# Performance work log

Hardware: AMD Instinct MI355X
Metric: run time of the kernel (lower is better)

## Reference

```python
import jax, jax.numpy as jnp
import numpy as np

P_FACTOR = 3.0
EPS = 1e-12  # torch F.normalize eps


def _l2_normalize(x):
    # matches torch.nn.functional.normalize(x, dim=-1): x / max(||x||, eps)
    n = jnp.linalg.norm(x, axis=-1, keepdims=True)
    return x / jnp.maximum(n, EPS)


def setup_inputs() -> dict:
    key = jax.random.key(0)
    k1, k2, k3 = jax.random.split(key, 3)
    N, D, H, C = 8192, 16384, 256, 28
    return {
        "features": jax.random.normal(k1, (N, H), dtype=jnp.float32),
        "ex_features": jax.random.normal(k2, (D, H), dtype=jnp.float32),
        "ex_class_reps": jax.random.normal(k3, (D, C), dtype=jnp.float32),
    }


def reference(features, ex_features, ex_class_reps):
    # cosine similarity: [N, D]
    s = _l2_normalize(features) @ _l2_normalize(ex_features).T
    # power-law activation: |s|^p * sign(s)
    a = jnp.power(jnp.abs(s), P_FACTOR) * jnp.sign(s)
    intensity = a.sum(axis=1)               # [N]
    echo = a @ ex_class_reps                # [N, C]
    return (echo, intensity)
```

## Files before the change

### kernel.cpp

```cpp
#include <hip/hip_runtime.h>
#include <stdint.h>


typedef unsigned short u16;
typedef __bf16 bf16x8 __attribute__((ext_vector_type(8)));
typedef float f32x4 __attribute__((ext_vector_type(4)));
typedef unsigned short u16x4 __attribute__((ext_vector_type(4)));

#define NQ 8192
#define ND 16384
#define NH 256
#define NC 28
#define DCHUNK 2048
#define NDT 32
#define NSLOT 8

__device__ __forceinline__ u16 f2bf(float f) {
  unsigned u = __builtin_bit_cast(unsigned, f);
  u += 0x7fffu + ((u >> 16) & 1u);
  return (u16)(u >> 16);
}

__device__ __forceinline__ unsigned cvtpk(float lo, float hi) {
  unsigned r;
  asm("v_cvt_pk_bf16_f32 %0, %1, %2" : "=v"(r) : "v"(lo), "v"(hi));
  return r;
}

__device__ __forceinline__ void swap2(unsigned& x, unsigned& y) {
  asm("v_permlane32_swap_b32 %0, %1" : "+v"(x), "+v"(y));
  asm("v_permlane16_swap_b32 %0, %1" : "+v"(x), "+v"(y));
}

__device__ __forceinline__ void gload16(const void* g, void* l) {
  __builtin_amdgcn_global_load_lds(
      (__attribute__((address_space(1))) void*)g,
      (__attribute__((address_space(3))) void*)l, 16, 0, 0);
}

__global__ __launch_bounds__(256) void prep_kernel(
    const float* __restrict__ feat, const float* __restrict__ exf,
    const float* __restrict__ V, u16* __restrict__ qn, u16* __restrict__ kn,
    u16* __restrict__ Vt) {
  if (blockIdx.x < 6144) {
    const int wid = threadIdx.x >> 6, lane = threadIdx.x & 63;
    const int row = blockIdx.x * 4 + wid;
    const float* in = (row < NQ) ? feat + (size_t)row * NH
                                 : exf + (size_t)(row - NQ) * NH;
    u16* out = (row < NQ) ? qn + (size_t)row * NH : kn + (size_t)(row - NQ) * NH;
    float4 v = ((const float4*)in)[lane];
    float ss = v.x * v.x + v.y * v.y + v.z * v.z + v.w * v.w;
#pragma unroll
    for (int m = 1; m <= 32; m <<= 1) ss += __shfl_xor(ss, m, 64);
    const float sc = 1.0f / fmaxf(sqrtf(ss), 1e-12f);
    u16x4 o;
    o.x = f2bf(v.x * sc); o.y = f2bf(v.y * sc);
    o.z = f2bf(v.z * sc); o.w = f2bf(v.w * sc);
    *(u16x4*)(out + lane * 4) = o;
  } else {
    const int d = (blockIdx.x - 6144) * 256 + threadIdx.x;
#pragma unroll
    for (int c = 0; c < NC; ++c) Vt[(size_t)c * ND + d] = f2bf(V[(size_t)d * NC + c]);
    Vt[(size_t)28 * ND + d] = 0x3F80;
    Vt[(size_t)29 * ND + d] = 0;
    Vt[(size_t)30 * ND + d] = 0;
    Vt[(size_t)31 * ND + d] = 0;
  }
}

__global__ __launch_bounds__(256, 3) void fused_kernel(
    const u16* __restrict__ Qn, const u16* __restrict__ Kn,
    const u16* __restrict__ Vt, float* __restrict__ ep) {
  __shared__ alignas(16) char smem[32768];
  const int tid = threadIdx.x;
  const int wid = tid >> 6;
  const int lane = tid & 63;
  const int l16 = lane & 15;
  const int lg = lane >> 4;
  const int dch = blockIdx.x & 7;
  const int ntile = blockIdx.x >> 3;
  const int rowbase = ntile * 128 + wid * 32;

  bf16x8 qA[2][8];
#pragma unroll
  for (int mb = 0; mb < 2; ++mb)
#pragma unroll
    for (int ks = 0; ks < 8; ++ks)
      qA[mb][ks] = *(const bf16x8*)(Qn + (size_t)(rowbase + mb * 16 + l16) * NH +
                                    ks * 32 + lg * 8);

  f32x4 eacc[2][2];
#pragma unroll
  for (int mb = 0; mb < 2; ++mb) {
    eacc[mb][0] = f32x4{0.f, 0.f, 0.f, 0.f};
    eacc[mb][1] = f32x4{0.f, 0.f, 0.f, 0.f};
  }
  f32x4 sacc[2][4];

  const u16* kc = Kn + (size_t)dch * DCHUNK * NH;
  const int srow = (tid >> 6) * 16 + ((tid >> 2) & 15);
  const u16* kb = kc + (size_t)srow * NH + ((tid & 3) ^ ((tid >> 3) & 3)) * 8;

  auto stage = [&](int buf, const u16* src0) {
#pragma unroll
    for (int r = 0; r < 4; ++r)
      gload16(src0 + r * 32,
              smem + buf * 16384 + r * 4096 + wid * 1024);
  };

  const int rsw = (l16 >> 1) & 3;

  auto compute = [&](int buf, int h) {
    const char* kbuf = smem + buf * 16384;
#pragma unroll
    for (int k2 = 0; k2 < 4; ++k2) {
      bf16x8 B[4];
#pragma unroll
      for (int nb = 0; nb < 4; ++nb)
        B[nb] = *(const bf16x8*)(kbuf + k2 * 4096 + (nb * 16 + l16) * 64 +
                                 ((lg ^ rsw) << 4));
      __builtin_amdgcn_s_setprio(1);
#pragma unroll
      for (int mb = 0; mb < 2; ++mb)
#pragma unroll
        for (int nb = 0; nb < 4; ++nb)
          sacc[mb][nb] = __builtin_amdgcn_mfma_f32_16x16x32_bf16(
              B[nb], qA[mb][h * 4 + k2], sacc[mb][nb], 0, 0, 0);
      __builtin_amdgcn_s_setprio(0);
    }
  };

  stage(0, kb);
  __syncthreads();

  for (int t = 0; t < NDT; ++t) {
    const size_t toff = (size_t)t * 64 * NH;
    const int dbase = dch * DCHUNK + t * 64;

    bf16x8 vB[2][2];
#pragma unroll
    for (int tg = 0; tg < 2; ++tg)
#pragma unroll
      for (int cn = 0; cn < 2; ++cn)
        vB[tg][cn] = *(const bf16x8*)(Vt + (size_t)(cn * 16 + l16) * ND +
                                      dbase + tg * 32 + lg * 8);

#pragma unroll
    for (int mb = 0; mb < 2; ++mb)
#pragma unroll
      for (int nb = 0; nb < 4; ++nb) sacc[mb][nb] = f32x4{0.f, 0.f, 0.f, 0.f};

    stage(1, kb + toff + 128);
    compute(0, 0);
    __syncthreads();
    if (t < NDT - 1) stage(0, kb + toff + 64 * NH);
    compute(1, 1);
    __syncthreads();

#pragma unroll
    for (int mb = 0; mb < 2; ++mb) {
#pragma unroll
      for (int tg = 0; tg < 2; ++tg) {
        f32x4 sx = sacc[mb][2 * tg];
        f32x4 sy = sacc[mb][2 * tg + 1];
        f32x4 cx = sx * sx * sx;
        f32x4 cy = sy * sy * sy;
        unsigned x0 = cvtpk(cx[0], cx[1]);
        unsigned x1 = cvtpk(cx[2], cx[3]);
        unsigned y0 = cvtpk(cy[0], cy[1]);
        unsigned y1 = cvtpk(cy[2], cy[3]);
        swap2(x0, y0);
        swap2(x1, y1);
        const int4 ai = {(int)x0, (int)x1, (int)y0, (int)y1};
        const bf16x8 aA = __builtin_bit_cast(bf16x8, ai);
#pragma unroll
        for (int cn = 0; cn < 2; ++cn)
          eacc[mb][cn] = __builtin_amdgcn_mfma_f32_16x16x32_bf16(
              aA, vB[tg][cn], eacc[mb][cn], 0, 0, 0);
      }
    }
  }

#pragma unroll
  for (int mb = 0; mb < 2; ++mb)
#pragma unroll
    for (int cn = 0; cn < 2; ++cn)
#pragma unroll
      for (int r = 0; r < 4; ++r) {
        const int row = rowbase + mb * 16 + lg * 4 + r;
        ep[((size_t)dch * NQ + row) * 32 + cn * 16 + l16] = eacc[mb][cn][r];
      }
}

__global__ __launch_bounds__(256) void reduce_kernel(const float* __restrict__ ep,
                                                     float* __restrict__ out) {
  const int g = blockIdx.x * 256 + threadIdx.x;
  const int q = g >> 5, c = g & 31;
  if (c < NC) {
    float s = 0.f;
#pragma unroll
    for (int k = 0; k < NSLOT; ++k) s += ep[((size_t)k * NQ + q) * 32 + c];
    out[(size_t)q * NC + c] = s;
  } else if (c == NC) {
    float s = 0.f;
#pragma unroll
    for (int k = 0; k < NSLOT; ++k) s += ep[((size_t)k * NQ + q) * 32 + NC];
    out[(size_t)NQ * NC + q] = s;
  }
}

extern "C" void kernel_launch(void* const* d_in, const int* in_sizes, int n_in,
                              void* d_out, int out_size, void* d_ws, size_t ws_size,
                              hipStream_t stream) {
  const float* feat = (const float*)d_in[0];
  const float* exf  = (const float*)d_in[1];
  const float* exc  = (const float*)d_in[2];
  float* out = (float*)d_out;
  char* ws = (char*)d_ws;
  u16* qn = (u16*)ws;
  u16* kn = (u16*)(ws + 4194304);
  u16* vt = (u16*)(ws + 12582912);
  float* ep = (float*)(ws + 13631488);

  prep_kernel<<<dim3(6208), dim3(256), 0, stream>>>(feat, exf, exc, qn, kn, vt);
  fused_kernel<<<dim3(512), dim3(256), 0, stream>>>(qn, kn, vt, ep);
  reduce_kernel<<<dim3(NQ * 32 / 256), dim3(256), 0, stream>>>(ep, out);
}
```

Measured before the change: 86.85 us.

## Split waves 2x2 over rows and key columns, merging echo partials via LDS

Each wave now covers 64 query rows and 32 of the 64 key columns per tile, instead of 32 rows and all 64 columns. Each B fragment read from LDS therefore feeds four MFMAs instead of two, which halves LDS reads per MFMA, and each wave loads only half of the V tile. The two column-half waves' echo accumulators are summed through shared memory before the global store. In exchange the per-thread Q fragments double to 64 VGPRs, so launch bounds drop to 2 blocks per CU, which lowers occupancy.

```diff
diff --git a/kernel.cpp b/kernel.cpp
--- a/kernel.cpp
+++ b/kernel.cpp
@@ -68,7 +68,7 @@
   }
 }
 
-__global__ __launch_bounds__(256, 3) void fused_kernel(
+__global__ __launch_bounds__(256, 2) void fused_kernel(
     const u16* __restrict__ Qn, const u16* __restrict__ Kn,
     const u16* __restrict__ Vt, float* __restrict__ ep) {
   __shared__ alignas(16) char smem[32768];
@@ -77,25 +77,27 @@
   const int lane = tid & 63;
   const int l16 = lane & 15;
   const int lg = lane >> 4;
+  const int wr = wid >> 1;
+  const int wd = wid & 1;
   const int dch = blockIdx.x & 7;
   const int ntile = blockIdx.x >> 3;
-  const int rowbase = ntile * 128 + wid * 32;
-
-  bf16x8 qA[2][8];
-#pragma unroll
-  for (int mb = 0; mb < 2; ++mb)
+  const int rowbase = ntile * 128 + wr * 64;
+
+  bf16x8 qA[4][8];
+#pragma unroll
+  for (int mb = 0; mb < 4; ++mb)
 #pragma unroll
     for (int ks = 0; ks < 8; ++ks)
       qA[mb][ks] = *(const bf16x8*)(Qn + (size_t)(rowbase + mb * 16 + l16) * NH +
                                     ks * 32 + lg * 8);
 
-  f32x4 eacc[2][2];
-#pragma unroll
-  for (int mb = 0; mb < 2; ++mb) {
+  f32x4 eacc[4][2];
+#pragma unroll
+  for (int mb = 0; mb < 4; ++mb) {
     eacc[mb][0] = f32x4{0.f, 0.f, 0.f, 0.f};
     eacc[mb][1] = f32x4{0.f, 0.f, 0.f, 0.f};
   }
-  f32x4 sacc[2][4];
+  f32x4 sacc[4][2];
 
   const u16* kc = Kn + (size_t)dch * DCHUNK * NH;
   const int srow = (tid >> 6) * 16 + ((tid >> 2) & 15);
@@ -114,16 +116,16 @@
     const char* kbuf = smem + buf * 16384;
 #pragma unroll
     for (int k2 = 0; k2 < 4; ++k2) {
-      bf16x8 B[4];
-#pragma unroll
-      for (int nb = 0; nb < 4; ++nb)
-        B[nb] = *(const bf16x8*)(kbuf + k2 * 4096 + (nb * 16 + l16) * 64 +
+      bf16x8 B[2];
+#pragma unroll
+      for (int nb = 0; nb < 2; ++nb)
+        B[nb] = *(const bf16x8*)(kbuf + k2 * 4096 + (wd * 32 + nb * 16 + l16) * 64 +
                                  ((lg ^ rsw) << 4));
       __builtin_amdgcn_s_setprio(1);
 #pragma unroll
-      for (int mb = 0; mb < 2; ++mb)
-#pragma unroll
-        for (int nb = 0; nb < 4; ++nb)
+      for (int mb = 0; mb < 4; ++mb)
+#pragma unroll
+        for (int nb = 0; nb < 2; ++nb)
           sacc[mb][nb] = __builtin_amdgcn_mfma_f32_16x16x32_bf16(
               B[nb], qA[mb][h * 4 + k2], sacc[mb][nb], 0, 0, 0);
       __builtin_amdgcn_s_setprio(0);
@@ -135,20 +137,18 @@
 
   for (int t = 0; t < NDT; ++t) {
     const size_t toff = (size_t)t * 64 * NH;
-    const int dbase = dch * DCHUNK + t * 64;
-
-    bf16x8 vB[2][2];
-#pragma unroll
-    for (int tg = 0; tg < 2; ++tg)
-#pragma unroll
-      for (int cn = 0; cn < 2; ++cn)
-        vB[tg][cn] = *(const bf16x8*)(Vt + (size_t)(cn * 16 + l16) * ND +
-                                      dbase + tg * 32 + lg * 8);
-
-#pragma unroll
-    for (int mb = 0; mb < 2; ++mb)
-#pragma unroll
-      for (int nb = 0; nb < 4; ++nb) sacc[mb][nb] = f32x4{0.f, 0.f, 0.f, 0.f};
+    const int dbase = dch * DCHUNK + t * 64 + wd * 32;
+
+    bf16x8 vB[2];
+#pragma unroll
+    for (int cn = 0; cn < 2; ++cn)
+      vB[cn] = *(const bf16x8*)(Vt + (size_t)(cn * 16 + l16) * ND + dbase + lg * 8);
+
+#pragma unroll
+    for (int mb = 0; mb < 4; ++mb) {
+      sacc[mb][0] = f32x4{0.f, 0.f, 0.f, 0.f};
+      sacc[mb][1] = f32x4{0.f, 0.f, 0.f, 0.f};
+    }
 
     stage(1, kb + toff + 128);
     compute(0, 0);
@@ -158,38 +158,50 @@
     __syncthreads();
 
 #pragma unroll
-    for (int mb = 0; mb < 2; ++mb) {
-#pragma unroll
-      for (int tg = 0; tg < 2; ++tg) {
-        f32x4 sx = sacc[mb][2 * tg];
-        f32x4 sy = sacc[mb][2 * tg + 1];
-        f32x4 cx = sx * sx * sx;
-        f32x4 cy = sy * sy * sy;
-        unsigned x0 = cvtpk(cx[0], cx[1]);
-        unsigned x1 = cvtpk(cx[2], cx[3]);
-        unsigned y0 = cvtpk(cy[0], cy[1]);
-        unsigned y1 = cvtpk(cy[2], cy[3]);
-        swap2(x0, y0);
-        swap2(x1, y1);
-        const int4 ai = {(int)x0, (int)x1, (int)y0, (int)y1};
-        const bf16x8 aA = __builtin_bit_cast(bf16x8, ai);
-#pragma unroll
-        for (int cn = 0; cn < 2; ++cn)
-          eacc[mb][cn] = __builtin_amdgcn_mfma_f32_16x16x32_bf16(
-              aA, vB[tg][cn], eacc[mb][cn], 0, 0, 0);
+    for (int mb = 0; mb < 4; ++mb) {
+      f32x4 sx = sacc[mb][0];
+      f32x4 sy = sacc[mb][1];
+      f32x4 cx = sx * sx * sx;
+      f32x4 cy = sy * sy * sy;
+      unsigned x0 = cvtpk(cx[0], cx[1]);
+      unsigned x1 = cvtpk(cx[2], cx[3]);
+      unsigned y0 = cvtpk(cy[0], cy[1]);
+      unsigned y1 = cvtpk(cy[2], cy[3]);
+      swap2(x0, y0);
+      swap2(x1, y1);
+      const int4 ai = {(int)x0, (int)x1, (int)y0, (int)y1};
+      const bf16x8 aA = __builtin_bit_cast(bf16x8, ai);
+#pragma unroll
+      for (int cn = 0; cn < 2; ++cn)
+        eacc[mb][cn] = __builtin_amdgcn_mfma_f32_16x16x32_bf16(
+            aA, vB[cn], eacc[mb][cn], 0, 0, 0);
+    }
+  }
+
+  float* eml = (float*)smem;
+  if (wd == 1) {
+    float* dst = eml + (wr * 64 + lane) * 36;
+#pragma unroll
+    for (int mb = 0; mb < 4; ++mb)
+#pragma unroll
+      for (int cn = 0; cn < 2; ++cn)
+        *(f32x4*)(dst + (mb * 2 + cn) * 4) = eacc[mb][cn];
+  }
+  __syncthreads();
+  if (wd == 0) {
+    const float* src = eml + (wr * 64 + lane) * 36;
+#pragma unroll
+    for (int mb = 0; mb < 4; ++mb)
+#pragma unroll
+      for (int cn = 0; cn < 2; ++cn) {
+        const f32x4 m = eacc[mb][cn] + *(const f32x4*)(src + (mb * 2 + cn) * 4);
+#pragma unroll
+        for (int r = 0; r < 4; ++r) {
+          const int row = rowbase + mb * 16 + lg * 4 + r;
+          ep[((size_t)dch * NQ + row) * 32 + cn * 16 + l16] = m[r];
+        }
       }
-    }
-  }
-
-#pragma unroll
-  for (int mb = 0; mb < 2; ++mb)
-#pragma unroll
-    for (int cn = 0; cn < 2; ++cn)
-#pragma unroll
-      for (int r = 0; r < 4; ++r) {
-        const int row = rowbase + mb * 16 + lg * 4 + r;
-        ep[((size_t)dch * NQ + row) * 32 + cn * 16 + l16] = eacc[mb][cn][r];
-      }
+  }
 }
 
 __global__ __launch_bounds__(256) void reduce_kernel(const float* __restrict__ ep,
```

Measured after the change: 82.92 us. 1.05x faster.
